# Optimization experiments

Measured on AMD Instinct MI355X. Metric: run time of the kernel, lower is better.

## Reference

```python
import jax, jax.numpy as jnp
import numpy as np

B = 32; D = 192; DEPTH = 4; DI = 384; DS = 16; DC = 4; P = 16; IMG = 224; N = 196; NC = 2


def setup_inputs() -> dict:
    key = jax.random.key(0)
    ks = iter(jax.random.split(key, 20))
    rn = lambda shape, s=0.02: jax.random.normal(next(ks), shape, dtype=jnp.float32) * s
    inp = {}
    inp["x"] = jax.random.normal(next(ks), (B, 3, IMG, IMG), dtype=jnp.float32)
    inp["patch_w"] = rn((D, 3 * P * P)); inp["patch_b"] = jnp.zeros((D,), jnp.float32)
    inp["cls_token"] = rn((1, 1, D)); inp["pos_embed"] = rn((1, N + 1, D))
    inp["ln_g"] = jnp.ones((DEPTH, D), jnp.float32); inp["ln_b"] = jnp.zeros((DEPTH, D), jnp.float32)
    inp["w_in"] = rn((DEPTH, 2 * DI, D))
    inp["conv_w"] = rn((DEPTH, DI, DC)); inp["conv_b"] = jnp.zeros((DEPTH, DI), jnp.float32)
    inp["w_x"] = rn((DEPTH, 2 * DS + 1, DI))
    inp["w_dt"] = rn((DEPTH, DI)); inp["b_dt"] = jnp.zeros((DEPTH, DI), jnp.float32)
    A = jnp.tile(jnp.arange(1, DS + 1, dtype=jnp.float32)[None, None, :], (DEPTH, DI, 1))
    inp["A_log"] = jnp.log(A)
    inp["D_ssm"] = jnp.ones((DEPTH, DI), jnp.float32)
    inp["w_out"] = rn((DEPTH, D, DI))
    inp["fn_g"] = jnp.ones((D,), jnp.float32); inp["fn_b"] = jnp.zeros((D,), jnp.float32)
    inp["cls_w"] = rn((NC, D)); inp["cls_b"] = jnp.zeros((NC,), jnp.float32)
    inp["reg_w1"] = rn((D // 2, D)); inp["reg_b1"] = jnp.zeros((D // 2,), jnp.float32)
    inp["reg_w2"] = rn((1, D // 2)); inp["reg_b2"] = jnp.zeros((1,), jnp.float32)
    return inp


def _ln(x, g, b):
    m = x.mean(-1, keepdims=True)
    v = ((x - m) ** 2).mean(-1, keepdims=True)
    return (x - m) / jnp.sqrt(v + 1e-5) * g + b


def _mamba(x, w_in, conv_w, conv_b, w_x, w_dt, b_dt, A_log, D_ssm, w_out):
    Bb, L, _ = x.shape
    xz = jnp.einsum('bld,ed->ble', x, w_in)           # [B,L,2*DI]
    xc, z = xz[..., :DI], xz[..., DI:]
    # causal depthwise conv1d (torch pads both sides then slices [:L] -> left-pad DC-1)
    xct = jnp.transpose(xc, (0, 2, 1))                 # [B,DI,L]
    xpad = jnp.pad(xct, ((0, 0), (0, 0), (DC - 1, 0)))
    conv = sum(conv_w[:, k, None] * xpad[:, :, k:k + L] for k in range(DC)) + conv_b[:, None]
    xa = jax.nn.silu(jnp.transpose(conv, (0, 2, 1)))   # [B,L,DI]
    bcd = jnp.einsum('bld,nd->bln', xa, w_x)           # [B,L,2*DS+1]
    Bm = bcd[..., :DS]; Cm = bcd[..., DS:2 * DS]
    dt = jax.nn.softplus(bcd[..., -1:] * w_dt + b_dt)  # [B,L,DI]  (Linear(1,DI))
    A = -jnp.exp(A_log)                                # [DI,DS]
    dA = jnp.exp(dt[..., None] * A)                    # [B,L,DI,DS]
    dBx = dt[..., None] * Bm[:, :, None, :] * xa[..., None]

    def step(h, inp):
        dA_t, dBx_t, C_t = inp
        h = dA_t * h + dBx_t
        return h, jnp.einsum('bdn,bn->bd', h, C_t)

    h0 = jnp.zeros((Bb, DI, DS), dtype=x.dtype)
    _, ys = jax.lax.scan(step, h0, (dA.transpose(1, 0, 2, 3), dBx.transpose(1, 0, 2, 3), Cm.transpose(1, 0, 2)))
    y = jnp.transpose(ys, (1, 0, 2)) + xa * D_ssm
    return jnp.einsum('bli,di->bld', y * jax.nn.silu(z), w_out)


def reference(x, patch_w, patch_b, cls_token, pos_embed, ln_g, ln_b, w_in, conv_w, conv_b,
              w_x, w_dt, b_dt, A_log, D_ssm, w_out, fn_g, fn_b, cls_w, cls_b,
              reg_w1, reg_b1, reg_w2, reg_b2):
    Bb = x.shape[0]
    H = IMG // P
    # non-overlapping patchify == Conv2d(kernel=stride=P)
    patches = x.reshape(Bb, 3, H, P, H, P).transpose(0, 2, 4, 1, 3, 5).reshape(Bb, N, 3 * P * P)
    tok = patches @ patch_w.T + patch_b
    t = jnp.concatenate([jnp.broadcast_to(cls_token, (Bb, 1, D)), tok], axis=1) + pos_embed
    for i in range(DEPTH):
        t = t + _mamba(_ln(t, ln_g[i], ln_b[i]), w_in[i], conv_w[i], conv_b[i],
                       w_x[i], w_dt[i], b_dt[i], A_log[i], D_ssm[i], w_out[i])
    feat = _ln(t, fn_g, fn_b)[:, 0]
    cls = feat @ cls_w.T + cls_b
    reg = jax.nn.gelu(feat @ reg_w1.T + reg_b1, approximate=False) @ reg_w2.T + reg_b2
    return (cls, reg)
```

## Files before the change

### kernel.cpp

```cpp
#include <hip/hip_runtime.h>
#include <hip/hip_bf16.h>
#include <math.h>

#define B_ 32
#define D_ 192
#define DEPTH_ 4
#define DI_ 384
#define DS_ 16
#define DC_ 4
#define P_ 16
#define IMG_ 224
#define N_ 196
#define L_ 197

#define NCH 16
#define CHL 13

typedef short s16x8 __attribute__((ext_vector_type(8)));
typedef float f32x16 __attribute__((ext_vector_type(16)));

__device__ __forceinline__ float sigmoidf_(float x) { return 1.f / (1.f + expf(-x)); }

__global__ __launch_bounds__(256) void k_prep(const float* __restrict__ patch_w,
                                              const float* __restrict__ w_in,
                                              const float* __restrict__ w_out,
                                              const float* __restrict__ w_x,
                                              const float* __restrict__ cls_tok,
                                              const float* __restrict__ pos,
                                              const float* __restrict__ A_log,
                                              __hip_bfloat16* __restrict__ pw,
                                              __hip_bfloat16* __restrict__ win,
                                              __hip_bfloat16* __restrict__ wout,
                                              __hip_bfloat16* __restrict__ wx,
                                              float* __restrict__ t,
                                              float* __restrict__ Aneg) {
  int idx = blockIdx.x * 256 + threadIdx.x;
  if (idx < 147456) { pw[idx] = __float2bfloat16(patch_w[idx]); return; }
  idx -= 147456;
  if (idx < 589824) { win[idx] = __float2bfloat16(w_in[idx]); return; }
  idx -= 589824;
  if (idx < 294912) { wout[idx] = __float2bfloat16(w_out[idx]); return; }
  idx -= 294912;
  if (idx < 98304) {
    int li = idx / 24576;
    int r = (idx / 384) & 63;
    int c = idx % 384;
    wx[idx] = (r < 33) ? __float2bfloat16(w_x[(li * 33 + r) * 384 + c]) : __float2bfloat16(0.f);
    return;
  }
  idx -= 98304;
  if (idx < 6144) {
    int b = idx / 192, d = idx % 192;
    t[(size_t)b * L_ * D_ + d] = cls_tok[d] + pos[d];
    return;
  }
  idx -= 6144;
  Aneg[idx] = -expf(A_log[idx]);
}

__global__ __launch_bounds__(256) void k_im2col(const float* __restrict__ x,
                                                __hip_bfloat16* __restrict__ A) {
  int idx = blockIdx.x * 256 + threadIdx.x;
  int tok = idx / 768, f = idx - tok * 768;
  int b = tok / 196, p = tok - b * 196;
  int h = p / 14, w = p - h * 14;
  int c = f >> 8, i = (f >> 4) & 15, j = f & 15;
  float v = x[(((size_t)(b * 3 + c) * 224 + h * 16 + i) * 224 + w * 16 + j)];
  A[idx] = __float2bfloat16(v);
}

template <int KTOT, int MODE>
__global__ __launch_bounds__(256) void k_gemm_mfma(const short* __restrict__ A,
                                                   const short* __restrict__ Wb,
                                                   float* __restrict__ C,
                                                   const float* __restrict__ bias,
                                                   const float* __restrict__ pos,
                                                   int M) {
  constexpr int KC = 96;
  constexpr int STR = 104;
  __shared__ __align__(16) short Als[64 * STR];
  __shared__ __align__(16) short Bls[64 * STR];
  int m0 = blockIdx.x * 64, n0 = blockIdx.y * 64;
  int tid = threadIdx.x;
  int lane = tid & 63, wid = tid >> 6;
  int mw = (wid & 1) * 32, nw = (wid >> 1) * 32;
  int l31 = lane & 31, lh = lane >> 5;
  f32x16 acc;
#pragma unroll
  for (int i = 0; i < 16; i++) acc[i] = 0.f;
  for (int kc = 0; kc < KTOT; kc += KC) {
    __syncthreads();
#pragma unroll
    for (int i = 0; i < 3; i++) {
      int seg = tid + i * 256;
      int r = seg / 12, s = seg - r * 12;
      *(s16x8*)(Als + r * STR + s * 8) =
          *(const s16x8*)(A + (size_t)(m0 + r) * KTOT + kc + s * 8);
      *(s16x8*)(Bls + r * STR + s * 8) =
          *(const s16x8*)(Wb + (size_t)(n0 + r) * KTOT + kc + s * 8);
    }
    __syncthreads();
#pragma unroll
    for (int ks = 0; ks < KC / 16; ks++) {
      s16x8 af = *(const s16x8*)(Als + (mw + l31) * STR + ks * 16 + lh * 8);
      s16x8 bf = *(const s16x8*)(Bls + (nw + l31) * STR + ks * 16 + lh * 8);
      acc = __builtin_amdgcn_mfma_f32_32x32x16_bf16(af, bf, acc, 0, 0, 0);
    }
  }
  int gn = n0 + nw + l31;
#pragma unroll
  for (int i = 0; i < 16; i++) {
    int rowt = mw + (i & 3) + 8 * (i >> 2) + 4 * lh;
    int gm = m0 + rowt;
    float v = acc[i];
    if (MODE == 1) {
      if (gm < M) C[(size_t)gm * 192 + gn] += v;
    } else if (MODE == 3) {
      if (gm < M) C[(size_t)gm * 64 + gn] = v;
    } else if (MODE == 4) {
      if (gm < M) ((__hip_bfloat16*)C)[(size_t)gm * 768 + gn] = __float2bfloat16(v);
    } else {
      int b = gm / 196, p = gm - b * 196;
      C[((size_t)b * 197 + 1 + p) * 192 + gn] =
          v + bias[gn] + pos[(size_t)(1 + p) * 192 + gn];
    }
  }
}

__global__ __launch_bounds__(256) void k_ln_bf(const float* __restrict__ t,
                                               const float* __restrict__ g,
                                               const float* __restrict__ bb,
                                               __hip_bfloat16* __restrict__ o) {
  int tok = blockIdx.x * 4 + (threadIdx.x >> 6);
  int tid = threadIdx.x & 63;
  const float* xr = t + (size_t)tok * D_;
  float x0 = xr[tid], x1 = xr[tid + 64], x2 = xr[tid + 128];
  float s = x0 + x1 + x2;
  float q = x0 * x0 + x1 * x1 + x2 * x2;
#pragma unroll
  for (int off = 1; off < 64; off <<= 1) {
    s += __shfl_xor(s, off, 64);
    q += __shfl_xor(q, off, 64);
  }
  float m = s * (1.f / 192.f);
  float r = rsqrtf(q * (1.f / 192.f) - m * m + 1e-5f);
  __hip_bfloat16* orow = o + (size_t)tok * D_;
  orow[tid]       = __float2bfloat16((x0 - m) * r * g[tid]       + bb[tid]);
  orow[tid + 64]  = __float2bfloat16((x1 - m) * r * g[tid + 64]  + bb[tid + 64]);
  orow[tid + 128] = __float2bfloat16((x2 - m) * r * g[tid + 128] + bb[tid + 128]);
}

__global__ __launch_bounds__(384) void k_conv(const __hip_bfloat16* __restrict__ xz,
                                              const float* __restrict__ cw_,
                                              const float* __restrict__ cb,
                                              __hip_bfloat16* __restrict__ xa_bf,
                                              __hip_bfloat16* __restrict__ sz_bf) {
  __shared__ float xs[11][384];
  int r0 = blockIdx.x * 8;
  int d = threadIdx.x;
#pragma unroll
  for (int row = 0; row < 11; row++) {
    int gr = r0 - 3 + row;
    if (gr >= 0) xs[row][d] = __bfloat162float(xz[(size_t)gr * 768 + d]);
  }
  __syncthreads();
  float4 cw = *(const float4*)(cw_ + d * 4);
  float cbv = cb[d];
#pragma unroll
  for (int tk = 0; tk < 8; tk++) {
    int tok = r0 + tk;
    int l = tok % L_;
    float acc = fmaf(cw.w, xs[tk + 3][d], cbv);
    if (l >= 1) acc = fmaf(cw.z, xs[tk + 2][d], acc);
    if (l >= 2) acc = fmaf(cw.y, xs[tk + 1][d], acc);
    if (l >= 3) acc = fmaf(cw.x, xs[tk][d], acc);
    float xav = acc * sigmoidf_(acc);
    xa_bf[(size_t)tok * DI_ + d] = __float2bfloat16(xav);
    float z = __bfloat162float(xz[(size_t)tok * 768 + 384 + d]);
    sz_bf[(size_t)tok * DI_ + d] = __float2bfloat16(z * sigmoidf_(z));
  }
}

__global__ __launch_bounds__(384) void k_scan1(const __hip_bfloat16* __restrict__ xa,
                                               const float* __restrict__ bcd,
                                               const float* __restrict__ Aneg,
                                               const float* __restrict__ w_dt,
                                               const float* __restrict__ b_dt,
                                               float* __restrict__ Sst,
                                               float* __restrict__ Hst) {
  int b = blockIdx.x >> 4, ch = blockIdx.x & 15;
  int d = threadIdx.x;
  int l0 = ch * CHL;
  int lim = min(CHL, L_ - l0);
  float Av[16];
#pragma unroll
  for (int q = 0; q < 4; q++) {
    float4 v = *(const float4*)(Aneg + d * 16 + q * 4);
    Av[q * 4] = v.x; Av[q * 4 + 1] = v.y; Av[q * 4 + 2] = v.z; Av[q * 4 + 3] = v.w;
  }
  float wdt = w_dt[d], bdt = b_dt[d];
  const __hip_bfloat16* xap = xa + ((size_t)b * L_ + l0) * DI_ + d;
  const float* bp = bcd + ((size_t)b * L_ + l0) * 64;
  float h[16];
  float Ssum = 0.f;
#pragma unroll
  for (int n = 0; n < 16; n++) h[n] = 0.f;
  float xv = __bfloat162float(xap[0]);
  for (int j = 0; j < lim; j++) {
    int jn = (j + 1 < lim) ? (j + 1) : j;
    float xn = __bfloat162float(xap[(size_t)jn * DI_]);
    float dtraw = bp[j * 64 + 32];
    float Bn[16];
#pragma unroll
    for (int n = 0; n < 16; n++) Bn[n] = bp[j * 64 + n];
    float v = fmaf(dtraw, wdt, bdt);
    float dtv = (v > 20.f) ? v : __logf(1.f + __expf(v));
    float dtx = dtv * xv;
    Ssum += dtv;
#pragma unroll
    for (int n = 0; n < 16; n++) {
      float dA = __expf(dtv * Av[n]);
      h[n] = fmaf(dA, h[n], dtx * Bn[n]);
    }
    xv = xn;
  }
  Sst[(size_t)blockIdx.x * 384 + d] = Ssum;
  size_t s = ((size_t)blockIdx.x * 384 + d) * 16;
#pragma unroll
  for (int q = 0; q < 4; q++) {
    *(float4*)(Hst + s + q * 4) = make_float4(h[q * 4], h[q * 4 + 1], h[q * 4 + 2], h[q * 4 + 3]);
  }
}

__global__ __launch_bounds__(256) void k_scan_mid(const float* __restrict__ Sst,
                                                  const float* __restrict__ Hst,
                                                  const float* __restrict__ Aneg,
                                                  float* __restrict__ Hinit) {
  int idx = blockIdx.x * 256 + threadIdx.x;
  int b = idx / 6144, r = idx - b * 6144;
  int d = r >> 4;
  float Av = Aneg[r];
  float h = 0.f;
#pragma unroll
  for (int c = 0; c < NCH; c++) {
    size_t o = (size_t)(b * NCH + c) * 6144 + r;
    float S = Sst[(size_t)(b * NCH + c) * 384 + d];
    Hinit[o] = h;
    h = fmaf(__expf(Av * S), h, Hst[o]);
  }
}

__global__ __launch_bounds__(384) void k_scan2(const __hip_bfloat16* __restrict__ xa,
                                               const __hip_bfloat16* __restrict__ sz,
                                               const float* __restrict__ bcd,
                                               const float* __restrict__ Aneg,
                                               const float* __restrict__ D_ssm,
                                               const float* __restrict__ w_dt,
                                               const float* __restrict__ b_dt,
                                               const float* __restrict__ Hinit,
                                               __hip_bfloat16* __restrict__ y) {
  int b = blockIdx.x >> 4, ch = blockIdx.x & 15;
  int d = threadIdx.x;
  int l0 = ch * CHL;
  int lim = min(CHL, L_ - l0);
  float Av[16];
#pragma unroll
  for (int q = 0; q < 4; q++) {
    float4 v = *(const float4*)(Aneg + d * 16 + q * 4);
    Av[q * 4] = v.x; Av[q * 4 + 1] = v.y; Av[q * 4 + 2] = v.z; Av[q * 4 + 3] = v.w;
  }
  float Dv = D_ssm[d];
  float wdt = w_dt[d], bdt = b_dt[d];
  const __hip_bfloat16* xap = xa + ((size_t)b * L_ + l0) * DI_ + d;
  const __hip_bfloat16* szp = sz + ((size_t)b * L_ + l0) * DI_ + d;
  const float* bp = bcd + ((size_t)b * L_ + l0) * 64;
  __hip_bfloat16* yp = y + ((size_t)b * L_ + l0) * DI_ + d;
  float h[16];
  {
    size_t s = ((size_t)blockIdx.x * 384 + d) * 16;
#pragma unroll
    for (int q = 0; q < 4; q++) {
      float4 v = *(const float4*)(Hinit + s + q * 4);
      h[q * 4] = v.x; h[q * 4 + 1] = v.y; h[q * 4 + 2] = v.z; h[q * 4 + 3] = v.w;
    }
  }
  float xv = __bfloat162float(xap[0]);
  float szv = __bfloat162float(szp[0]);
  for (int j = 0; j < lim; j++) {
    int jn = (j + 1 < lim) ? (j + 1) : j;
    float xn = __bfloat162float(xap[(size_t)jn * DI_]);
    float szn = __bfloat162float(szp[(size_t)jn * DI_]);
    float dtraw = bp[j * 64 + 32];
    float Bn[16], Cn[16];
#pragma unroll
    for (int n = 0; n < 16; n++) Bn[n] = bp[j * 64 + n];
#pragma unroll
    for (int n = 0; n < 16; n++) Cn[n] = bp[j * 64 + 16 + n];
    float v = fmaf(dtraw, wdt, bdt);
    float dtv = (v > 20.f) ? v : __logf(1.f + __expf(v));
    float dtx = dtv * xv;
    float acc = 0.f;
#pragma unroll
    for (int n = 0; n < 16; n++) {
      float dA = __expf(dtv * Av[n]);
      h[n] = fmaf(dA, h[n], dtx * Bn[n]);
      acc = fmaf(h[n], Cn[n], acc);
    }
    float yv = fmaf(xv, Dv, acc) * szv;
    yp[(size_t)j * DI_] = __float2bfloat16(yv);
    xv = xn; szv = szn;
  }
}

__global__ __launch_bounds__(192) void k_head(const float* __restrict__ t,
                                              const float* __restrict__ fn_g,
                                              const float* __restrict__ fn_b,
                                              const float* __restrict__ cls_w,
                                              const float* __restrict__ cls_b,
                                              const float* __restrict__ rw1,
                                              const float* __restrict__ rb1,
                                              const float* __restrict__ rw2,
                                              const float* __restrict__ rb2,
                                              float* __restrict__ out) {
  __shared__ float red[8];
  __shared__ float stats[2];
  __shared__ float feat_s[192];
  __shared__ float h_s[96];
  int b = blockIdx.x, tid = threadIdx.x;
  float x = t[(size_t)b * L_ * D_ + tid];
  float s = x, q = x * x;
#pragma unroll
  for (int off = 1; off < 64; off <<= 1) {
    s += __shfl_xor(s, off, 64);
    q += __shfl_xor(q, off, 64);
  }
  int w = tid >> 6;
  if ((tid & 63) == 0) { red[w] = s; red[4 + w] = q; }
  __syncthreads();
  if (tid == 0) {
    float ss = red[0] + red[1] + red[2];
    float qq = red[4] + red[5] + red[6];
    float m = ss * (1.f / 192.f);
    stats[0] = m;
    stats[1] = rsqrtf(qq * (1.f / 192.f) - m * m + 1e-5f);
  }
  __syncthreads();
  float fv = (x - stats[0]) * stats[1] * fn_g[tid] + fn_b[tid];
  feat_s[tid] = fv;
  __syncthreads();
  if (tid < 96) {
    float a = rb1[tid];
    const float* wr = rw1 + (size_t)tid * 192;
    for (int k = 0; k < 192; k++) a = fmaf(feat_s[k], wr[k], a);
    h_s[tid] = 0.5f * a * (1.f + erff(a * 0.70710678118654752f));
  } else if (tid < 98) {
    int c = tid - 96;
    float a = cls_b[c];
    const float* wr = cls_w + (size_t)c * 192;
    for (int k = 0; k < 192; k++) a = fmaf(feat_s[k], wr[k], a);
    out[b * 2 + c] = a;
  }
  __syncthreads();
  if (tid == 0) {
    float a = rb2[0];
    for (int j = 0; j < 96; j++) a = fmaf(h_s[j], rw2[j], a);
    out[64 + b] = a;
  }
}

extern "C" void kernel_launch(void* const* d_in, const int* in_sizes, int n_in,
                              void* d_out, int out_size, void* d_ws, size_t ws_size,
                              hipStream_t stream) {
  const float* x       = (const float*)d_in[0];
  const float* patch_w = (const float*)d_in[1];
  const float* patch_b = (const float*)d_in[2];
  const float* cls_tok = (const float*)d_in[3];
  const float* pos     = (const float*)d_in[4];
  const float* ln_g    = (const float*)d_in[5];
  const float* ln_b    = (const float*)d_in[6];
  const float* w_in    = (const float*)d_in[7];
  const float* conv_w  = (const float*)d_in[8];
  const float* conv_b  = (const float*)d_in[9];
  const float* w_x     = (const float*)d_in[10];
  const float* w_dt    = (const float*)d_in[11];
  const float* b_dt    = (const float*)d_in[12];
  const float* A_log   = (const float*)d_in[13];
  const float* D_ssm   = (const float*)d_in[14];
  const float* w_out   = (const float*)d_in[15];
  const float* fn_g    = (const float*)d_in[16];
  const float* fn_b    = (const float*)d_in[17];
  const float* cls_w   = (const float*)d_in[18];
  const float* cls_b   = (const float*)d_in[19];
  const float* reg_w1  = (const float*)d_in[20];
  const float* reg_b1  = (const float*)d_in[21];
  const float* reg_w2  = (const float*)d_in[22];
  const float* reg_b2  = (const float*)d_in[23];
  float* out = (float*)d_out;

  float* ws = (float*)d_ws;
  float* t_buf = ws;
  float* bcd   = t_buf + 1210368;
  float* Sst   = bcd + 405504;
  float* Hst   = Sst + 3145728;
  float* Hinit = Hst + 3145728;
  float* Aneg  = Hinit + 3145728;
  __hip_bfloat16* xz_bf  = (__hip_bfloat16*)(Aneg + 24576);
  __hip_bfloat16* Abuf   = xz_bf;
  __hip_bfloat16* xa_bf  = xz_bf + 4841472;
  __hip_bfloat16* sz_bf  = xa_bf + 2433024;
  __hip_bfloat16* xln_bf = sz_bf + 2433024;
  __hip_bfloat16* y_bf   = xln_bf + 1216512;
  __hip_bfloat16* pw_bf  = y_bf + 2433024;
  __hip_bfloat16* win_bf = pw_bf + 147456;
  __hip_bfloat16* wout_bf = win_bf + 589824;
  __hip_bfloat16* wx_bf  = wout_bf + 294912;

  k_prep<<<4536, 256, 0, stream>>>(patch_w, w_in, w_out, w_x, cls_tok, pos, A_log,
                                   pw_bf, win_bf, wout_bf, wx_bf, t_buf, Aneg);
  k_im2col<<<18816, 256, 0, stream>>>(x, Abuf);
  k_gemm_mfma<768, 2><<<dim3(98, 3), 256, 0, stream>>>(
      (const short*)Abuf, (const short*)pw_bf, t_buf, patch_b, pos, 6272);

  for (int i = 0; i < DEPTH_; i++) {
    k_ln_bf<<<1576, 256, 0, stream>>>(t_buf, ln_g + i * D_, ln_b + i * D_, xln_bf);
    k_gemm_mfma<192, 4><<<dim3(99, 12), 256, 0, stream>>>(
        (const short*)xln_bf, (const short*)(win_bf + (size_t)i * 147456), (float*)xz_bf,
        nullptr, nullptr, 6304);
    k_conv<<<788, 384, 0, stream>>>(xz_bf, conv_w + i * DI_ * DC_, conv_b + i * DI_,
                                    xa_bf, sz_bf);
    k_gemm_mfma<384, 3><<<dim3(99, 1), 256, 0, stream>>>(
        (const short*)xa_bf, (const short*)(wx_bf + (size_t)i * 24576), bcd,
        nullptr, nullptr, 6304);
    k_scan1<<<B_ * NCH, 384, 0, stream>>>(xa_bf, bcd, Aneg + i * 6144,
                                          w_dt + i * DI_, b_dt + i * DI_, Sst, Hst);
    k_scan_mid<<<768, 256, 0, stream>>>(Sst, Hst, Aneg + i * 6144, Hinit);
    k_scan2<<<B_ * NCH, 384, 0, stream>>>(xa_bf, sz_bf, bcd, Aneg + i * 6144,
                                          D_ssm + i * DI_, w_dt + i * DI_, b_dt + i * DI_,
                                          Hinit, y_bf);
    k_gemm_mfma<384, 1><<<dim3(99, 3), 256, 0, stream>>>(
        (const short*)y_bf, (const short*)(wout_bf + (size_t)i * 73728), t_buf,
        nullptr, nullptr, 6304);
  }
  k_head<<<32, 192, 0, stream>>>(t_buf, fn_g, fn_b, cls_w, cls_b, reg_w1, reg_b1,
                                 reg_w2, reg_b2, out);
}
```

Measured before the change: 436.2 us.

## Fuse three-pass chunked scan into one cooperative kernel with grid sync

Replaces the scan1 / scan_mid / scan2 kernel sequence with a single cooperative-launch kernel. Chunk-local states are computed, a grid-wide sync follows, and then each block recombines the prefix of earlier chunk states itself before running the output pass. This removes two kernel launches per layer and the Hinit buffer round trip. In exchange it adds a grid barrier and redundant per-block prefix work of up to 15 chunks, and it requires all 512 blocks of 384 threads to be co-resident.

```diff
diff --git a/kernel.cpp b/kernel.cpp
--- a/kernel.cpp
+++ b/kernel.cpp
@@ -1,6 +1,9 @@
 #include <hip/hip_runtime.h>
 #include <hip/hip_bf16.h>
+#include <hip/hip_cooperative_groups.h>
 #include <math.h>
+
+namespace cg = cooperative_groups;
 
 #define B_ 32
 #define D_ 192
@@ -181,13 +184,16 @@
   }
 }
 
-__global__ __launch_bounds__(384) void k_scan1(const __hip_bfloat16* __restrict__ xa,
-                                               const float* __restrict__ bcd,
-                                               const float* __restrict__ Aneg,
-                                               const float* __restrict__ w_dt,
-                                               const float* __restrict__ b_dt,
-                                               float* __restrict__ Sst,
-                                               float* __restrict__ Hst) {
+__global__ __launch_bounds__(384) void k_scan_fused(const __hip_bfloat16* __restrict__ xa,
+                                                    const __hip_bfloat16* __restrict__ sz,
+                                                    const float* __restrict__ bcd,
+                                                    const float* __restrict__ Aneg,
+                                                    const float* __restrict__ D_ssm,
+                                                    const float* __restrict__ w_dt,
+                                                    const float* __restrict__ b_dt,
+                                                    float* __restrict__ Sst,
+                                                    float* __restrict__ Hst,
+                                                    __hip_bfloat16* __restrict__ y) {
   int b = blockIdx.x >> 4, ch = blockIdx.x & 15;
   int d = threadIdx.x;
   int l0 = ch * CHL;
@@ -201,89 +207,61 @@
   float wdt = w_dt[d], bdt = b_dt[d];
   const __hip_bfloat16* xap = xa + ((size_t)b * L_ + l0) * DI_ + d;
   const float* bp = bcd + ((size_t)b * L_ + l0) * 64;
+
+  {
+    float h[16];
+    float Ssum = 0.f;
+#pragma unroll
+    for (int n = 0; n < 16; n++) h[n] = 0.f;
+    float xv = __bfloat162float(xap[0]);
+    for (int j = 0; j < lim; j++) {
+      int jn = (j + 1 < lim) ? (j + 1) : j;
+      float xn = __bfloat162float(xap[(size_t)jn * DI_]);
+      float dtraw = bp[j * 64 + 32];
+      float Bn[16];
+#pragma unroll
+      for (int n = 0; n < 16; n++) Bn[n] = bp[j * 64 + n];
+      float v = fmaf(dtraw, wdt, bdt);
+      float dtv = (v > 20.f) ? v : __logf(1.f + __expf(v));
+      float dtx = dtv * xv;
+      Ssum += dtv;
+#pragma unroll
+      for (int n = 0; n < 16; n++) {
+        float dA = __expf(dtv * Av[n]);
+        h[n] = fmaf(dA, h[n], dtx * Bn[n]);
+      }
+      xv = xn;
+    }
+    Sst[(size_t)blockIdx.x * 384 + d] = Ssum;
+    size_t s = ((size_t)blockIdx.x * 384 + d) * 16;
+#pragma unroll
+    for (int q = 0; q < 4; q++) {
+      *(float4*)(Hst + s + q * 4) =
+          make_float4(h[q * 4], h[q * 4 + 1], h[q * 4 + 2], h[q * 4 + 3]);
+    }
+  }
+  __threadfence();
+  cg::this_grid().sync();
+
   float h[16];
-  float Ssum = 0.f;
 #pragma unroll
   for (int n = 0; n < 16; n++) h[n] = 0.f;
-  float xv = __bfloat162float(xap[0]);
-  for (int j = 0; j < lim; j++) {
-    int jn = (j + 1 < lim) ? (j + 1) : j;
-    float xn = __bfloat162float(xap[(size_t)jn * DI_]);
-    float dtraw = bp[j * 64 + 32];
-    float Bn[16];
-#pragma unroll
-    for (int n = 0; n < 16; n++) Bn[n] = bp[j * 64 + n];
-    float v = fmaf(dtraw, wdt, bdt);
-    float dtv = (v > 20.f) ? v : __logf(1.f + __expf(v));
-    float dtx = dtv * xv;
-    Ssum += dtv;
-#pragma unroll
-    for (int n = 0; n < 16; n++) {
-      float dA = __expf(dtv * Av[n]);
-      h[n] = fmaf(dA, h[n], dtx * Bn[n]);
-    }
-    xv = xn;
-  }
-  Sst[(size_t)blockIdx.x * 384 + d] = Ssum;
-  size_t s = ((size_t)blockIdx.x * 384 + d) * 16;
-#pragma unroll
-  for (int q = 0; q < 4; q++) {
-    *(float4*)(Hst + s + q * 4) = make_float4(h[q * 4], h[q * 4 + 1], h[q * 4 + 2], h[q * 4 + 3]);
-  }
-}
-
-__global__ __launch_bounds__(256) void k_scan_mid(const float* __restrict__ Sst,
-                                                  const float* __restrict__ Hst,
-                                                  const float* __restrict__ Aneg,
-                                                  float* __restrict__ Hinit) {
-  int idx = blockIdx.x * 256 + threadIdx.x;
-  int b = idx / 6144, r = idx - b * 6144;
-  int d = r >> 4;
-  float Av = Aneg[r];
-  float h = 0.f;
-#pragma unroll
-  for (int c = 0; c < NCH; c++) {
-    size_t o = (size_t)(b * NCH + c) * 6144 + r;
-    float S = Sst[(size_t)(b * NCH + c) * 384 + d];
-    Hinit[o] = h;
-    h = fmaf(__expf(Av * S), h, Hst[o]);
-  }
-}
-
-__global__ __launch_bounds__(384) void k_scan2(const __hip_bfloat16* __restrict__ xa,
-                                               const __hip_bfloat16* __restrict__ sz,
-                                               const float* __restrict__ bcd,
-                                               const float* __restrict__ Aneg,
-                                               const float* __restrict__ D_ssm,
-                                               const float* __restrict__ w_dt,
-                                               const float* __restrict__ b_dt,
-                                               const float* __restrict__ Hinit,
-                                               __hip_bfloat16* __restrict__ y) {
-  int b = blockIdx.x >> 4, ch = blockIdx.x & 15;
-  int d = threadIdx.x;
-  int l0 = ch * CHL;
-  int lim = min(CHL, L_ - l0);
-  float Av[16];
-#pragma unroll
-  for (int q = 0; q < 4; q++) {
-    float4 v = *(const float4*)(Aneg + d * 16 + q * 4);
-    Av[q * 4] = v.x; Av[q * 4 + 1] = v.y; Av[q * 4 + 2] = v.z; Av[q * 4 + 3] = v.w;
-  }
+  for (int c = 0; c < ch; c++) {
+    size_t base = ((size_t)(b * NCH + c) * 384 + d);
+    float S = Sst[base];
+    float Hc[16];
+#pragma unroll
+    for (int q = 0; q < 4; q++) {
+      float4 v = *(const float4*)(Hst + base * 16 + q * 4);
+      Hc[q * 4] = v.x; Hc[q * 4 + 1] = v.y; Hc[q * 4 + 2] = v.z; Hc[q * 4 + 3] = v.w;
+    }
+#pragma unroll
+    for (int n = 0; n < 16; n++) h[n] = fmaf(__expf(Av[n] * S), h[n], Hc[n]);
+  }
+
   float Dv = D_ssm[d];
-  float wdt = w_dt[d], bdt = b_dt[d];
-  const __hip_bfloat16* xap = xa + ((size_t)b * L_ + l0) * DI_ + d;
   const __hip_bfloat16* szp = sz + ((size_t)b * L_ + l0) * DI_ + d;
-  const float* bp = bcd + ((size_t)b * L_ + l0) * 64;
   __hip_bfloat16* yp = y + ((size_t)b * L_ + l0) * DI_ + d;
-  float h[16];
-  {
-    size_t s = ((size_t)blockIdx.x * 384 + d) * 16;
-#pragma unroll
-    for (int q = 0; q < 4; q++) {
-      float4 v = *(const float4*)(Hinit + s + q * 4);
-      h[q * 4] = v.x; h[q * 4 + 1] = v.y; h[q * 4 + 2] = v.z; h[q * 4 + 3] = v.w;
-    }
-  }
   float xv = __bfloat162float(xap[0]);
   float szv = __bfloat162float(szp[0]);
   for (int j = 0; j < lim; j++) {
@@ -431,12 +409,22 @@
     k_gemm_mfma<384, 3><<<dim3(99, 1), 256, 0, stream>>>(
         (const short*)xa_bf, (const short*)(wx_bf + (size_t)i * 24576), bcd,
         nullptr, nullptr, 6304);
-    k_scan1<<<B_ * NCH, 384, 0, stream>>>(xa_bf, bcd, Aneg + i * 6144,
-                                          w_dt + i * DI_, b_dt + i * DI_, Sst, Hst);
-    k_scan_mid<<<768, 256, 0, stream>>>(Sst, Hst, Aneg + i * 6144, Hinit);
-    k_scan2<<<B_ * NCH, 384, 0, stream>>>(xa_bf, sz_bf, bcd, Aneg + i * 6144,
-                                          D_ssm + i * DI_, w_dt + i * DI_, b_dt + i * DI_,
-                                          Hinit, y_bf);
+    {
+      const __hip_bfloat16* xa_p = xa_bf;
+      const __hip_bfloat16* sz_p = sz_bf;
+      const float* bcd_p = bcd;
+      const float* An_p  = Aneg + i * 6144;
+      const float* D_p   = D_ssm + i * DI_;
+      const float* wdt_p = w_dt + i * DI_;
+      const float* bdt_p = b_dt + i * DI_;
+      float* Sst_p = Sst;
+      float* Hst_p = Hst;
+      __hip_bfloat16* y_p = y_bf;
+      void* args[] = {&xa_p, &sz_p, &bcd_p, &An_p, &D_p, &wdt_p, &bdt_p,
+                      &Sst_p, &Hst_p, &y_p};
+      hipLaunchCooperativeKernel((const void*)k_scan_fused, dim3(B_ * NCH), dim3(384),
+                                 args, 0, stream);
+    }
     k_gemm_mfma<384, 1><<<dim3(99, 3), 256, 0, stream>>>(
         (const short*)y_bf, (const short*)(wout_bf + (size_t)i * 73728), t_buf,
         nullptr, nullptr, 6304);
```

Result: slower. 1.164 ms (+166.7%).

## Fold chunk-prefix combine into scan2 and drop scan_mid kernel

Applied to the files above, without the earlier changes.

Removes the separate k_scan_mid launch that turned per-chunk summaries into initial states. Each k_scan2 block now rebuilds its own initial state by folding over all earlier chunks' (S, H) summaries. scan1 also skips the last chunk, since its summary is never used. This saves one launch and a Hinit write/read round trip per layer, at the cost of redundant prefix work (up to 15 chunks of 16 exps and loads per thread) in later-chunk blocks.

```diff
diff --git a/kernel.cpp b/kernel.cpp
--- a/kernel.cpp
+++ b/kernel.cpp
@@ -189,6 +189,7 @@
                                                float* __restrict__ Sst,
                                                float* __restrict__ Hst) {
   int b = blockIdx.x >> 4, ch = blockIdx.x & 15;
+  if (ch == 15) return;
   int d = threadIdx.x;
   int l0 = ch * CHL;
   int lim = min(CHL, L_ - l0);
@@ -232,24 +233,6 @@
   }
 }
 
-__global__ __launch_bounds__(256) void k_scan_mid(const float* __restrict__ Sst,
-                                                  const float* __restrict__ Hst,
-                                                  const float* __restrict__ Aneg,
-                                                  float* __restrict__ Hinit) {
-  int idx = blockIdx.x * 256 + threadIdx.x;
-  int b = idx / 6144, r = idx - b * 6144;
-  int d = r >> 4;
-  float Av = Aneg[r];
-  float h = 0.f;
-#pragma unroll
-  for (int c = 0; c < NCH; c++) {
-    size_t o = (size_t)(b * NCH + c) * 6144 + r;
-    float S = Sst[(size_t)(b * NCH + c) * 384 + d];
-    Hinit[o] = h;
-    h = fmaf(__expf(Av * S), h, Hst[o]);
-  }
-}
-
 __global__ __launch_bounds__(384) void k_scan2(const __hip_bfloat16* __restrict__ xa,
                                                const __hip_bfloat16* __restrict__ sz,
                                                const float* __restrict__ bcd,
@@ -257,7 +240,8 @@
                                                const float* __restrict__ D_ssm,
                                                const float* __restrict__ w_dt,
                                                const float* __restrict__ b_dt,
-                                               const float* __restrict__ Hinit,
+                                               const float* __restrict__ Sst,
+                                               const float* __restrict__ Hst,
                                                __hip_bfloat16* __restrict__ y) {
   int b = blockIdx.x >> 4, ch = blockIdx.x & 15;
   int d = threadIdx.x;
@@ -269,21 +253,27 @@
     float4 v = *(const float4*)(Aneg + d * 16 + q * 4);
     Av[q * 4] = v.x; Av[q * 4 + 1] = v.y; Av[q * 4 + 2] = v.z; Av[q * 4 + 3] = v.w;
   }
+  float h[16];
+#pragma unroll
+  for (int n = 0; n < 16; n++) h[n] = 0.f;
+  for (int c = 0; c < ch; c++) {
+    size_t base = ((size_t)(b * NCH + c) * 384 + d);
+    float S = Sst[base];
+    float Hc[16];
+#pragma unroll
+    for (int q = 0; q < 4; q++) {
+      float4 v = *(const float4*)(Hst + base * 16 + q * 4);
+      Hc[q * 4] = v.x; Hc[q * 4 + 1] = v.y; Hc[q * 4 + 2] = v.z; Hc[q * 4 + 3] = v.w;
+    }
+#pragma unroll
+    for (int n = 0; n < 16; n++) h[n] = fmaf(__expf(Av[n] * S), h[n], Hc[n]);
+  }
   float Dv = D_ssm[d];
   float wdt = w_dt[d], bdt = b_dt[d];
   const __hip_bfloat16* xap = xa + ((size_t)b * L_ + l0) * DI_ + d;
   const __hip_bfloat16* szp = sz + ((size_t)b * L_ + l0) * DI_ + d;
   const float* bp = bcd + ((size_t)b * L_ + l0) * 64;
   __hip_bfloat16* yp = y + ((size_t)b * L_ + l0) * DI_ + d;
-  float h[16];
-  {
-    size_t s = ((size_t)blockIdx.x * 384 + d) * 16;
-#pragma unroll
-    for (int q = 0; q < 4; q++) {
-      float4 v = *(const float4*)(Hinit + s + q * 4);
-      h[q * 4] = v.x; h[q * 4 + 1] = v.y; h[q * 4 + 2] = v.z; h[q * 4 + 3] = v.w;
-    }
-  }
   float xv = __bfloat162float(xap[0]);
   float szv = __bfloat162float(szp[0]);
   for (int j = 0; j < lim; j++) {
@@ -433,10 +423,9 @@
         nullptr, nullptr, 6304);
     k_scan1<<<B_ * NCH, 384, 0, stream>>>(xa_bf, bcd, Aneg + i * 6144,
                                           w_dt + i * DI_, b_dt + i * DI_, Sst, Hst);
-    k_scan_mid<<<768, 256, 0, stream>>>(Sst, Hst, Aneg + i * 6144, Hinit);
     k_scan2<<<B_ * NCH, 384, 0, stream>>>(xa_bf, sz_bf, bcd, Aneg + i * 6144,
                                           D_ssm + i * DI_, w_dt + i * DI_, b_dt + i * DI_,
-                                          Hinit, y_bf);
+                                          Sst, Hst, y_bf);
     k_gemm_mfma<384, 1><<<dim3(99, 3), 256, 0, stream>>>(
         (const short*)y_bf, (const short*)(wout_bf + (size_t)i * 73728), t_buf,
         nullptr, nullptr, 6304);
```

Result: slower. 464.4 us (+6.4%).

## Fuse im2col into patch GEMM, move z-silu into scan2, skip last chunk scan1

Applied to the files above, without the earlier changes.

Folds the im2col gather and bf16 conversion into the patch-embedding GEMM's shared-memory load, which removes a separate kernel and its intermediate buffer. The silu(z) gate is now computed inside scan2 from the xz buffer, so the conv kernel no longer writes the sz buffer. scan1 skips the final chunk because its end state is never consumed, and scan_mid is adjusted to match. The trade-off is strided float4 loads from the image inside the GEMM and extra sigmoid work in the sequential scan loop.

```diff
diff --git a/kernel.cpp b/kernel.cpp
--- a/kernel.cpp
+++ b/kernel.cpp
@@ -20,6 +20,10 @@
 typedef float f32x16 __attribute__((ext_vector_type(16)));
 
 __device__ __forceinline__ float sigmoidf_(float x) { return 1.f / (1.f + expf(-x)); }
+__device__ __forceinline__ short f2bf(float x) {
+  __hip_bfloat16 h = __float2bfloat16(x);
+  return *reinterpret_cast<short*>(&h);
+}
 
 __global__ __launch_bounds__(256) void k_prep(const float* __restrict__ patch_w,
                                               const float* __restrict__ w_in,
@@ -58,23 +62,67 @@
   Aneg[idx] = -expf(A_log[idx]);
 }
 
-__global__ __launch_bounds__(256) void k_im2col(const float* __restrict__ x,
-                                                __hip_bfloat16* __restrict__ A) {
-  int idx = blockIdx.x * 256 + threadIdx.x;
-  int tok = idx / 768, f = idx - tok * 768;
-  int b = tok / 196, p = tok - b * 196;
-  int h = p / 14, w = p - h * 14;
-  int c = f >> 8, i = (f >> 4) & 15, j = f & 15;
-  float v = x[(((size_t)(b * 3 + c) * 224 + h * 16 + i) * 224 + w * 16 + j)];
-  A[idx] = __float2bfloat16(v);
+__global__ __launch_bounds__(256) void k_gemm_patch(const float* __restrict__ x,
+                                                    const short* __restrict__ Wb,
+                                                    float* __restrict__ C,
+                                                    const float* __restrict__ bias,
+                                                    const float* __restrict__ pos) {
+  constexpr int KC = 96;
+  constexpr int STR = 104;
+  __shared__ __align__(16) short Als[64 * STR];
+  __shared__ __align__(16) short Bls[64 * STR];
+  int m0 = blockIdx.x * 64, n0 = blockIdx.y * 64;
+  int tid = threadIdx.x;
+  int lane = tid & 63, wid = tid >> 6;
+  int mw = (wid & 1) * 32, nw = (wid >> 1) * 32;
+  int l31 = lane & 31, lh = lane >> 5;
+  f32x16 acc;
+#pragma unroll
+  for (int i = 0; i < 16; i++) acc[i] = 0.f;
+  for (int kc = 0; kc < 768; kc += KC) {
+    __syncthreads();
+#pragma unroll
+    for (int i2 = 0; i2 < 3; i2++) {
+      int seg = tid + i2 * 256;
+      int r = seg / 12, s5 = seg - r * 12;
+      int k = kc + s5 * 8;
+      int c = k >> 8, rem = k & 255, ii = rem >> 4, jj = rem & 15;
+      int tok = m0 + r;
+      int b2 = tok / 196, p2 = tok - b2 * 196;
+      int hh = p2 / 14, ww = p2 - hh * 14;
+      const float* xp = x + (((size_t)(b2 * 3 + c) * 224 + hh * 16 + ii) * 224 + ww * 16 + jj);
+      float4 u0 = *(const float4*)xp;
+      float4 u1 = *(const float4*)(xp + 4);
+      s16x8 o;
+      o[0] = f2bf(u0.x); o[1] = f2bf(u0.y); o[2] = f2bf(u0.z); o[3] = f2bf(u0.w);
+      o[4] = f2bf(u1.x); o[5] = f2bf(u1.y); o[6] = f2bf(u1.z); o[7] = f2bf(u1.w);
+      *(s16x8*)(Als + r * STR + s5 * 8) = o;
+      *(s16x8*)(Bls + r * STR + s5 * 8) =
+          *(const s16x8*)(Wb + (size_t)(n0 + r) * 768 + kc + s5 * 8);
+    }
+    __syncthreads();
+#pragma unroll
+    for (int ks = 0; ks < KC / 16; ks++) {
+      s16x8 af = *(const s16x8*)(Als + (mw + l31) * STR + ks * 16 + lh * 8);
+      s16x8 bf = *(const s16x8*)(Bls + (nw + l31) * STR + ks * 16 + lh * 8);
+      acc = __builtin_amdgcn_mfma_f32_32x32x16_bf16(af, bf, acc, 0, 0, 0);
+    }
+  }
+  int gn = n0 + nw + l31;
+#pragma unroll
+  for (int i = 0; i < 16; i++) {
+    int rowt = mw + (i & 3) + 8 * (i >> 2) + 4 * lh;
+    int gm = m0 + rowt;
+    int b = gm / 196, p = gm - b * 196;
+    C[((size_t)b * 197 + 1 + p) * 192 + gn] =
+        acc[i] + bias[gn] + pos[(size_t)(1 + p) * 192 + gn];
+  }
 }
 
 template <int KTOT, int MODE>
 __global__ __launch_bounds__(256) void k_gemm_mfma(const short* __restrict__ A,
                                                    const short* __restrict__ Wb,
                                                    float* __restrict__ C,
-                                                   const float* __restrict__ bias,
-                                                   const float* __restrict__ pos,
                                                    int M) {
   constexpr int KC = 96;
   constexpr int STR = 104;
@@ -119,10 +167,6 @@
       if (gm < M) C[(size_t)gm * 64 + gn] = v;
     } else if (MODE == 4) {
       if (gm < M) ((__hip_bfloat16*)C)[(size_t)gm * 768 + gn] = __float2bfloat16(v);
-    } else {
-      int b = gm / 196, p = gm - b * 196;
-      C[((size_t)b * 197 + 1 + p) * 192 + gn] =
-          v + bias[gn] + pos[(size_t)(1 + p) * 192 + gn];
     }
   }
 }
@@ -153,8 +197,7 @@
 __global__ __launch_bounds__(384) void k_conv(const __hip_bfloat16* __restrict__ xz,
                                               const float* __restrict__ cw_,
                                               const float* __restrict__ cb,
-                                              __hip_bfloat16* __restrict__ xa_bf,
-                                              __hip_bfloat16* __restrict__ sz_bf) {
+                                              __hip_bfloat16* __restrict__ xa_bf) {
   __shared__ float xs[11][384];
   int r0 = blockIdx.x * 8;
   int d = threadIdx.x;
@@ -176,8 +219,6 @@
     if (l >= 3) acc = fmaf(cw.x, xs[tk][d], acc);
     float xav = acc * sigmoidf_(acc);
     xa_bf[(size_t)tok * DI_ + d] = __float2bfloat16(xav);
-    float z = __bfloat162float(xz[(size_t)tok * 768 + 384 + d]);
-    sz_bf[(size_t)tok * DI_ + d] = __float2bfloat16(z * sigmoidf_(z));
   }
 }
 
@@ -188,10 +229,10 @@
                                                const float* __restrict__ b_dt,
                                                float* __restrict__ Sst,
                                                float* __restrict__ Hst) {
-  int b = blockIdx.x >> 4, ch = blockIdx.x & 15;
+  int b = blockIdx.x / 15, ch = blockIdx.x % 15;
   int d = threadIdx.x;
   int l0 = ch * CHL;
-  int lim = min(CHL, L_ - l0);
+  int lim = CHL;
   float Av[16];
 #pragma unroll
   for (int q = 0; q < 4; q++) {
@@ -224,8 +265,9 @@
     }
     xv = xn;
   }
-  Sst[(size_t)blockIdx.x * 384 + d] = Ssum;
-  size_t s = ((size_t)blockIdx.x * 384 + d) * 16;
+  size_t sidx = (size_t)(b * NCH + ch) * 384 + d;
+  Sst[sidx] = Ssum;
+  size_t s = sidx * 16;
 #pragma unroll
   for (int q = 0; q < 4; q++) {
     *(float4*)(Hst + s + q * 4) = make_float4(h[q * 4], h[q * 4 + 1], h[q * 4 + 2], h[q * 4 + 3]);
@@ -242,16 +284,17 @@
   float Av = Aneg[r];
   float h = 0.f;
 #pragma unroll
-  for (int c = 0; c < NCH; c++) {
+  for (int c = 0; c < NCH - 1; c++) {
     size_t o = (size_t)(b * NCH + c) * 6144 + r;
     float S = Sst[(size_t)(b * NCH + c) * 384 + d];
     Hinit[o] = h;
     h = fmaf(__expf(Av * S), h, Hst[o]);
   }
+  Hinit[(size_t)(b * NCH + NCH - 1) * 6144 + r] = h;
 }
 
 __global__ __launch_bounds__(384) void k_scan2(const __hip_bfloat16* __restrict__ xa,
-                                               const __hip_bfloat16* __restrict__ sz,
+                                               const __hip_bfloat16* __restrict__ xz,
                                                const float* __restrict__ bcd,
                                                const float* __restrict__ Aneg,
                                                const float* __restrict__ D_ssm,
@@ -272,7 +315,7 @@
   float Dv = D_ssm[d];
   float wdt = w_dt[d], bdt = b_dt[d];
   const __hip_bfloat16* xap = xa + ((size_t)b * L_ + l0) * DI_ + d;
-  const __hip_bfloat16* szp = sz + ((size_t)b * L_ + l0) * DI_ + d;
+  const __hip_bfloat16* zp = xz + ((size_t)b * L_ + l0) * 768 + 384 + d;
   const float* bp = bcd + ((size_t)b * L_ + l0) * 64;
   __hip_bfloat16* yp = y + ((size_t)b * L_ + l0) * DI_ + d;
   float h[16];
@@ -285,11 +328,11 @@
     }
   }
   float xv = __bfloat162float(xap[0]);
-  float szv = __bfloat162float(szp[0]);
+  float zv = __bfloat162float(zp[0]);
   for (int j = 0; j < lim; j++) {
     int jn = (j + 1 < lim) ? (j + 1) : j;
     float xn = __bfloat162float(xap[(size_t)jn * DI_]);
-    float szn = __bfloat162float(szp[(size_t)jn * DI_]);
+    float zn = __bfloat162float(zp[(size_t)jn * 768]);
     float dtraw = bp[j * 64 + 32];
     float Bn[16], Cn[16];
 #pragma unroll
@@ -306,9 +349,10 @@
       h[n] = fmaf(dA, h[n], dtx * Bn[n]);
       acc = fmaf(h[n], Cn[n], acc);
     }
+    float szv = zv * sigmoidf_(zv);
     float yv = fmaf(xv, Dv, acc) * szv;
     yp[(size_t)j * DI_] = __float2bfloat16(yv);
-    xv = xn; szv = szn;
+    xv = xn; zv = zn;
   }
 }
 
@@ -405,7 +449,6 @@
   float* Hinit = Hst + 3145728;
   float* Aneg  = Hinit + 3145728;
   __hip_bfloat16* xz_bf  = (__hip_bfloat16*)(Aneg + 24576);
-  __hip_bfloat16* Abuf   = xz_bf;
   __hip_bfloat16* xa_bf  = xz_bf + 4841472;
   __hip_bfloat16* sz_bf  = xa_bf + 2433024;
   __hip_bfloat16* xln_bf = sz_bf + 2433024;
@@ -417,29 +460,26 @@
 
   k_prep<<<4536, 256, 0, stream>>>(patch_w, w_in, w_out, w_x, cls_tok, pos, A_log,
                                    pw_bf, win_bf, wout_bf, wx_bf, t_buf, Aneg);
-  k_im2col<<<18816, 256, 0, stream>>>(x, Abuf);
-  k_gemm_mfma<768, 2><<<dim3(98, 3), 256, 0, stream>>>(
-      (const short*)Abuf, (const short*)pw_bf, t_buf, patch_b, pos, 6272);
+  k_gemm_patch<<<dim3(98, 3), 256, 0, stream>>>(x, (const short*)pw_bf, t_buf,
+                                                patch_b, pos);
 
   for (int i = 0; i < DEPTH_; i++) {
     k_ln_bf<<<1576, 256, 0, stream>>>(t_buf, ln_g + i * D_, ln_b + i * D_, xln_bf);
     k_gemm_mfma<192, 4><<<dim3(99, 12), 256, 0, stream>>>(
         (const short*)xln_bf, (const short*)(win_bf + (size_t)i * 147456), (float*)xz_bf,
-        nullptr, nullptr, 6304);
+        6304);
     k_conv<<<788, 384, 0, stream>>>(xz_bf, conv_w + i * DI_ * DC_, conv_b + i * DI_,
-                                    xa_bf, sz_bf);
+                                    xa_bf);
     k_gemm_mfma<384, 3><<<dim3(99, 1), 256, 0, stream>>>(
-        (const short*)xa_bf, (const short*)(wx_bf + (size_t)i * 24576), bcd,
-        nullptr, nullptr, 6304);
-    k_scan1<<<B_ * NCH, 384, 0, stream>>>(xa_bf, bcd, Aneg + i * 6144,
-                                          w_dt + i * DI_, b_dt + i * DI_, Sst, Hst);
+        (const short*)xa_bf, (const short*)(wx_bf + (size_t)i * 24576), bcd, 6304);
+    k_scan1<<<B_ * (NCH - 1), 384, 0, stream>>>(xa_bf, bcd, Aneg + i * 6144,
+                                                w_dt + i * DI_, b_dt + i * DI_, Sst, Hst);
     k_scan_mid<<<768, 256, 0, stream>>>(Sst, Hst, Aneg + i * 6144, Hinit);
-    k_scan2<<<B_ * NCH, 384, 0, stream>>>(xa_bf, sz_bf, bcd, Aneg + i * 6144,
+    k_scan2<<<B_ * NCH, 384, 0, stream>>>(xa_bf, xz_bf, bcd, Aneg + i * 6144,
                                           D_ssm + i * DI_, w_dt + i * DI_, b_dt + i * DI_,
                                           Hinit, y_bf);
     k_gemm_mfma<384, 1><<<dim3(99, 3), 256, 0, stream>>>(
-        (const short*)y_bf, (const short*)(wout_bf + (size_t)i * 73728), t_buf,
-        nullptr, nullptr, 6304);
+        (const short*)y_bf, (const short*)(wout_bf + (size_t)i * 73728), t_buf, 6304);
   }
   k_head<<<32, 192, 0, stream>>>(t_buf, fn_g, fn_b, cls_w, cls_b, reg_w1, reg_b1,
                                  reg_w2, reg_b2, out);
```

Result: no change. 433.4 us (-0.6%).
